# Kernel tuning notes

Hardware: AMD Instinct MI355X
Metric: run time of the kernel (lower is better)

Reference implementation:

```python
import jax, jax.numpy as jnp
import numpy as np

N_NODES = 100000
DEG = 16          # regular-graph degree so degrees[start] > 0 for all nodes
STEPS = 32
D_FEAT = 16
MAXI32 = 2147483647


def setup_inputs() -> dict:
    key = jax.random.key(0)
    k1, k2, k3 = jax.random.split(key, 3)
    x = jax.random.normal(k1, (N_NODES, D_FEAT), dtype=jnp.float32)
    # CSR-style flat adjacency list: node v's neighbors are
    # adj_nodes[adj_offset[v] : adj_offset[v] + degrees[v]]
    adj_nodes = jax.random.randint(k2, (N_NODES * DEG,), 0, N_NODES, dtype=jnp.int32)
    adj_offset = (jnp.arange(N_NODES, dtype=jnp.int32) * DEG)
    degrees = jnp.full((N_NODES,), DEG, dtype=jnp.int32)
    # cache of random integers, one per (step, walk), as in the torch code
    choices = jax.random.randint(k3, (STEPS, N_NODES), 0, MAXI32, dtype=jnp.int32)
    return {"x": x, "adj_nodes": adj_nodes, "adj_offset": adj_offset,
            "degrees": degrees, "choices": choices}


def reference(x, adj_nodes, adj_offset, degrees, choices):
    """Non-backtracking random walk (Walker.sample_walks with start_p=1.0,
    all nodes having degree > 0, so start = arange(n)).
    Returns walks [steps+1, w] and walk_edges [steps, w]."""
    n = degrees.shape[0]
    nb_degrees = jnp.maximum(degrees - 1, 1)  # reduced degree for non-backtrack rewrite
    start = jnp.arange(n, dtype=jnp.int32)

    def step(carry, ch):
        prev, cur = carry                      # [w] previous / current nodes
        deg = degrees[cur]
        edge_idx = ch % deg                    # unweighted modulo edge choice
        chosen = adj_offset[cur] + edge_idx
        new = adj_nodes[chosen]
        bt = new == prev                       # backtracking walks
        # conditional rewrite: pick a different outgoing edge
        alt = adj_offset[cur] + (edge_idx + 1 + ch % nb_degrees[cur]) % deg
        chosen = jnp.where(bt, alt, chosen)
        new = jnp.where(bt, adj_nodes[alt], new)
        return (cur, new), (new, chosen)

    # prev = -1 at step 0 => bt is all-False, matching the i > 0 guard
    prev0 = jnp.full_like(start, -1)
    _, (nodes, walk_edges) = jax.lax.scan(step, (prev0, start), choices)
    walks = jnp.concatenate([start[None, :], nodes], axis=0)  # [steps+1, w]
    return walks, walk_edges
```

## Files before the change

### kernel.cpp

```cpp
#include <hip/hip_runtime.h>


#define DEG 16
#define CHAINS 2
#define NMAX 131072
#define PACK_BLOCK 256
#define ENT_MASK 0x3FFFFu

__device__ unsigned int g_pk32[(size_t)NMAX * 9 + 2];
__device__ int g_flag;

__global__ __launch_bounds__(PACK_BLOCK) void pack_check_kernel(
    const int* __restrict__ adj_nodes,
    const int* __restrict__ adj_offset,
    const int* __restrict__ degrees,
    int n, int epoch) {
    __shared__ __align__(16) unsigned int lds[PACK_BLOCK * 9];

    int tid = threadIdx.x;
    int blockStart = blockIdx.x * PACK_BLOCK;
    int v = blockStart + tid;

    bool bad = false;
    if (v < n) {
        bad = (degrees[v] != DEG) || (adj_offset[v] != v * DEG);

        const uint4* row4 = (const uint4*)(adj_nodes + (size_t)v * DEG);
        uint4 r[4];
        r[0] = row4[0]; r[1] = row4[1]; r[2] = row4[2]; r[3] = row4[3];
        const unsigned* rr = (const unsigned*)r;

        unsigned dw[9];
#pragma unroll
        for (int j = 0; j < 9; ++j) dw[j] = 0u;
#pragma unroll
        for (int e = 0; e < 16; ++e) {
            unsigned id = rr[e];
            if (id >= 262144u) bad = true;
            unsigned s   = 18u * (unsigned)e;
            unsigned d   = s >> 5;
            unsigned off = s & 31u;
            dw[d] |= id << off;
            if (off > 14u) dw[d + 1] |= id >> (32u - off);
        }
#pragma unroll
        for (int e = 0; e < 16; ++e) {
            unsigned s   = 18u * (unsigned)e;
            unsigned d   = s >> 5;
            unsigned off = s & 31u;
            unsigned hi  = (off > 14u) ? dw[d + 1] : 0u;
            unsigned id  = __builtin_amdgcn_alignbit(hi, dw[d], off) & ENT_MASK;
            if (id != rr[e]) bad = true;
        }
#pragma unroll
        for (int j = 0; j < 9; ++j) lds[tid * 9 + j] = dw[j];
    }
    __syncthreads();

    int rows = n - blockStart;
    if (rows > PACK_BLOCK) rows = PACK_BLOCK;
    unsigned int* dstBase = g_pk32 + (size_t)blockStart * 9;
    if (rows == PACK_BLOCK) {
        uint4* dst4 = (uint4*)dstBase;
        const uint4* src4 = (const uint4*)lds;
        for (int i = tid; i < (PACK_BLOCK * 9) / 4; i += PACK_BLOCK)
            dst4[i] = src4[i];
    } else {
        int ndw = rows * 9;
        for (int i = tid; i < ndw; i += PACK_BLOCK) dstBase[i] = lds[i];
    }

    if (bad) g_flag = epoch;
}

template <int STEPS>
__global__ __launch_bounds__(64) void walker_fast5(
    const int* __restrict__ choices,
    int* __restrict__ out, int n, int h, int epoch,
    const int* __restrict__ adj_nodes,
    const int* __restrict__ adj_offset,
    const int* __restrict__ degrees) {

    int t = blockIdx.x * blockDim.x + threadIdx.x;
    if (t >= h) return;

    int* walks      = out;
    int* walk_edges = out + (STEPS + 1) * n;

    int w0 = t;
    int w1 = t + h;
    bool has1 = (w1 < n);
    int w1s = has1 ? w1 : w0;

    __builtin_nontemporal_store(w0, &walks[w0]);
    if (has1) __builtin_nontemporal_store(w1, &walks[w1]);

    if (g_flag != epoch) {
        int c0[STEPS], c1[STEPS];
#pragma unroll
        for (int i = 0; i < STEPS; ++i) {
            c0[i] = __builtin_nontemporal_load(&choices[i * n + w0]);
            c1[i] = __builtin_nontemporal_load(&choices[i * n + w1s]);
        }

        int prev0 = -1, cur0 = w0;
        int prev1 = -1, cur1 = w1s;
#pragma unroll
        for (int i = 0; i < STEPS; ++i) {
            unsigned ch0 = (unsigned)c0[i];
            unsigned ch1 = (unsigned)c1[i];
            unsigned e0 = ch0 & (DEG - 1);
            unsigned e1 = ch1 & (DEG - 1);
            unsigned a0 = (e0 + 1u + ch0 % (DEG - 1)) & (DEG - 1);
            unsigned a1 = (e1 + 1u + ch1 % (DEG - 1)) & (DEG - 1);

            const unsigned* row0 = g_pk32 + (size_t)(unsigned)cur0 * 9u;
            const unsigned* row1 = g_pk32 + (size_t)(unsigned)cur1 * 9u;

            unsigned s0 = 18u * e0, d0 = s0 >> 5, f0 = s0 & 31u;
            unsigned s1 = 18u * e1, d1 = s1 >> 5, f1 = s1 & 31u;
            unsigned sa = 18u * a0, da = sa >> 5, fa = sa & 31u;
            unsigned sb = 18u * a1, db = sb >> 5, fb = sb & 31u;

            uint2 q0 = *(const uint2*)(row0 + d0);
            uint2 qa = *(const uint2*)(row0 + da);
            uint2 q1 = *(const uint2*)(row1 + d1);
            uint2 qb = *(const uint2*)(row1 + db);

            int n00 = (int)(__builtin_amdgcn_alignbit(q0.y, q0.x, f0) & ENT_MASK);
            int n0a = (int)(__builtin_amdgcn_alignbit(qa.y, qa.x, fa) & ENT_MASK);
            int n10 = (int)(__builtin_amdgcn_alignbit(q1.y, q1.x, f1) & ENT_MASK);
            int n1b = (int)(__builtin_amdgcn_alignbit(qb.y, qb.x, fb) & ENT_MASK);

            bool bt0 = (n00 == prev0);
            bool bt1 = (n10 == prev1);
            int nw0 = bt0 ? n0a : n00;
            int nw1 = bt1 ? n1b : n10;
            unsigned ef0 = bt0 ? a0 : e0;
            unsigned ef1 = bt1 ? a1 : e1;

            int ce0 = (cur0 << 4) + (int)ef0;
            int ce1 = (cur1 << 4) + (int)ef1;

            __builtin_nontemporal_store(nw0, &walks[(i + 1) * n + w0]);
            __builtin_nontemporal_store(ce0, &walk_edges[i * n + w0]);
            if (has1) {
                __builtin_nontemporal_store(nw1, &walks[(i + 1) * n + w1]);
                __builtin_nontemporal_store(ce1, &walk_edges[i * n + w1]);
            }
            prev0 = cur0; cur0 = nw0;
            prev1 = cur1; cur1 = nw1;
        }
    } else {
        for (int k = 0; k < 2; ++k) {
            int w = (k == 0) ? w0 : w1;
            if (w >= n) break;
            int prev = -1, cur = w;
            for (int i = 0; i < STEPS; ++i) {
                int chv = choices[i * n + w];
                int deg = degrees[cur];
                int off = adj_offset[cur];
                int nb  = deg - 1 > 1 ? deg - 1 : 1;

                int e      = chv % deg;
                int chosen = off + e;
                int alt    = off + (e + 1 + chv % nb) % deg;

                int nv0 = adj_nodes[chosen];
                int nv1 = adj_nodes[alt];

                bool bt = (nv0 == prev);
                int nw  = bt ? nv1 : nv0;
                walks[(i + 1) * n + w] = nw;
                walk_edges[i * n + w]  = bt ? alt : chosen;
                prev = cur;
                cur  = nw;
            }
        }
    }
}

__global__ __launch_bounds__(256) void walker_generic(
    const int* __restrict__ adj_nodes,
    const int* __restrict__ adj_offset,
    const int* __restrict__ degrees,
    const int* __restrict__ choices,
    int* __restrict__ out, int n, int steps) {

    int w = blockIdx.x * blockDim.x + threadIdx.x;
    if (w >= n) return;

    int* walks      = out;
    int* walk_edges = out + (steps + 1) * n;
    walks[w] = w;

    int prev = -1, cur = w;
    for (int i = 0; i < steps; ++i) {
        int chv = choices[i * n + w];
        int deg = degrees[cur];
        int off = adj_offset[cur];
        int nb  = deg - 1 > 1 ? deg - 1 : 1;

        int e      = chv % deg;
        int chosen = off + e;
        int alt    = off + (e + 1 + chv % nb) % deg;

        int nv0 = adj_nodes[chosen];
        int nv1 = adj_nodes[alt];

        bool bt = (nv0 == prev);
        int nw  = bt ? nv1 : nv0;
        walks[(i + 1) * n + w] = nw;
        walk_edges[i * n + w]  = bt ? alt : chosen;
        prev = cur;
        cur  = nw;
    }
}

extern "C" void kernel_launch(void* const* d_in, const int* in_sizes, int n_in,
                              void* d_out, int out_size, void* d_ws, size_t ws_size,
                              hipStream_t stream) {
    const int* adj_nodes  = (const int*)d_in[1];
    const int* adj_offset = (const int*)d_in[2];
    const int* degrees    = (const int*)d_in[3];
    const int* choices    = (const int*)d_in[4];
    int* out = (int*)d_out;

    int n     = in_sizes[2];
    int steps = in_sizes[4] / n;

    if (steps == 32 && n <= NMAX) {
        static int s_epoch = 0;
        int epoch = ++s_epoch;

        int pg = (n + PACK_BLOCK - 1) / PACK_BLOCK;
        pack_check_kernel<<<pg, PACK_BLOCK, 0, stream>>>(adj_nodes, adj_offset,
                                                         degrees, n, epoch);

        int h  = (n + CHAINS - 1) / CHAINS;
        int wb = 64, wg = (h + wb - 1) / wb;
        walker_fast5<32><<<wg, wb, 0, stream>>>(choices, out, n, h, epoch,
                                                adj_nodes, adj_offset, degrees);
    } else {
        int block = 256, grid = (n + block - 1) / block;
        walker_generic<<<grid, block, 0, stream>>>(adj_nodes, adj_offset,
                                                   degrees, choices, out, n, steps);
    }
}
```

Measured before the change: 105.4 us.

## Use one walk per thread with lazy alternate-edge load and rolling choice prefetch

Replaces the two-walks-per-thread kernel with one walk per thread in 256-thread blocks, doubling the thread count. Choices are no longer preloaded into a 32-entry register array; each step prefetches only the next one. The alternate-edge load and modulo-15 are now done only when the chosen neighbour equals the previous node. This cuts registers and redundant gathers to raise occupancy, but gives up the two independent dependency chains per thread that hid gather latency.

```diff
diff --git a/kernel.cpp b/kernel.cpp
--- a/kernel.cpp
+++ b/kernel.cpp
@@ -2,7 +2,6 @@
 
 
 #define DEG 16
-#define CHAINS 2
 #define NMAX 131072
 #define PACK_BLOCK 256
 #define ENT_MASK 0x3FFFFu
@@ -74,108 +73,72 @@
 }
 
 template <int STEPS>
-__global__ __launch_bounds__(64) void walker_fast5(
+__global__ __launch_bounds__(256) void walker_fast6(
     const int* __restrict__ choices,
-    int* __restrict__ out, int n, int h, int epoch,
+    int* __restrict__ out, int n, int epoch,
     const int* __restrict__ adj_nodes,
     const int* __restrict__ adj_offset,
     const int* __restrict__ degrees) {
 
-    int t = blockIdx.x * blockDim.x + threadIdx.x;
-    if (t >= h) return;
+    int w = blockIdx.x * blockDim.x + threadIdx.x;
+    if (w >= n) return;
 
     int* walks      = out;
     int* walk_edges = out + (STEPS + 1) * n;
 
-    int w0 = t;
-    int w1 = t + h;
-    bool has1 = (w1 < n);
-    int w1s = has1 ? w1 : w0;
-
-    __builtin_nontemporal_store(w0, &walks[w0]);
-    if (has1) __builtin_nontemporal_store(w1, &walks[w1]);
+    __builtin_nontemporal_store(w, &walks[w]);
 
     if (g_flag != epoch) {
-        int c0[STEPS], c1[STEPS];
+        int prev = -1, cur = w;
+        int ch_next = __builtin_nontemporal_load(&choices[w]);
 #pragma unroll
         for (int i = 0; i < STEPS; ++i) {
-            c0[i] = __builtin_nontemporal_load(&choices[i * n + w0]);
-            c1[i] = __builtin_nontemporal_load(&choices[i * n + w1s]);
-        }
-
-        int prev0 = -1, cur0 = w0;
-        int prev1 = -1, cur1 = w1s;
-#pragma unroll
+            unsigned ch = (unsigned)ch_next;
+            if (i + 1 < STEPS)
+                ch_next = __builtin_nontemporal_load(&choices[(i + 1) * n + w]);
+
+            unsigned e = ch & (DEG - 1);
+            const unsigned* row = g_pk32 + (size_t)(unsigned)cur * 9u;
+            unsigned s = 18u * e, d = s >> 5, f = s & 31u;
+
+            uint2 q = *(const uint2*)(row + d);
+            int cand = (int)(__builtin_amdgcn_alignbit(q.y, q.x, f) & ENT_MASK);
+
+            int nw = cand;
+            unsigned ef = e;
+            if (cand == prev) {
+                unsigned a  = (e + 1u + ch % (DEG - 1)) & (DEG - 1);
+                unsigned sa = 18u * a, da = sa >> 5, fa = sa & 31u;
+                uint2 qa = *(const uint2*)(row + da);
+                nw = (int)(__builtin_amdgcn_alignbit(qa.y, qa.x, fa) & ENT_MASK);
+                ef = a;
+            }
+
+            __builtin_nontemporal_store(nw, &walks[(i + 1) * n + w]);
+            __builtin_nontemporal_store((cur << 4) + (int)ef, &walk_edges[i * n + w]);
+            prev = cur; cur = nw;
+        }
+    } else {
+        int prev = -1, cur = w;
         for (int i = 0; i < STEPS; ++i) {
-            unsigned ch0 = (unsigned)c0[i];
-            unsigned ch1 = (unsigned)c1[i];
-            unsigned e0 = ch0 & (DEG - 1);
-            unsigned e1 = ch1 & (DEG - 1);
-            unsigned a0 = (e0 + 1u + ch0 % (DEG - 1)) & (DEG - 1);
-            unsigned a1 = (e1 + 1u + ch1 % (DEG - 1)) & (DEG - 1);
-
-            const unsigned* row0 = g_pk32 + (size_t)(unsigned)cur0 * 9u;
-            const unsigned* row1 = g_pk32 + (size_t)(unsigned)cur1 * 9u;
-
-            unsigned s0 = 18u * e0, d0 = s0 >> 5, f0 = s0 & 31u;
-            unsigned s1 = 18u * e1, d1 = s1 >> 5, f1 = s1 & 31u;
-            unsigned sa = 18u * a0, da = sa >> 5, fa = sa & 31u;
-            unsigned sb = 18u * a1, db = sb >> 5, fb = sb & 31u;
-
-            uint2 q0 = *(const uint2*)(row0 + d0);
-            uint2 qa = *(const uint2*)(row0 + da);
-            uint2 q1 = *(const uint2*)(row1 + d1);
-            uint2 qb = *(const uint2*)(row1 + db);
-
-            int n00 = (int)(__builtin_amdgcn_alignbit(q0.y, q0.x, f0) & ENT_MASK);
-            int n0a = (int)(__builtin_amdgcn_alignbit(qa.y, qa.x, fa) & ENT_MASK);
-            int n10 = (int)(__builtin_amdgcn_alignbit(q1.y, q1.x, f1) & ENT_MASK);
-            int n1b = (int)(__builtin_amdgcn_alignbit(qb.y, qb.x, fb) & ENT_MASK);
-
-            bool bt0 = (n00 == prev0);
-            bool bt1 = (n10 == prev1);
-            int nw0 = bt0 ? n0a : n00;
-            int nw1 = bt1 ? n1b : n10;
-            unsigned ef0 = bt0 ? a0 : e0;
-            unsigned ef1 = bt1 ? a1 : e1;
-
-            int ce0 = (cur0 << 4) + (int)ef0;
-            int ce1 = (cur1 << 4) + (int)ef1;
-
-            __builtin_nontemporal_store(nw0, &walks[(i + 1) * n + w0]);
-            __builtin_nontemporal_store(ce0, &walk_edges[i * n + w0]);
-            if (has1) {
-                __builtin_nontemporal_store(nw1, &walks[(i + 1) * n + w1]);
-                __builtin_nontemporal_store(ce1, &walk_edges[i * n + w1]);
-            }
-            prev0 = cur0; cur0 = nw0;
-            prev1 = cur1; cur1 = nw1;
-        }
-    } else {
-        for (int k = 0; k < 2; ++k) {
-            int w = (k == 0) ? w0 : w1;
-            if (w >= n) break;
-            int prev = -1, cur = w;
-            for (int i = 0; i < STEPS; ++i) {
-                int chv = choices[i * n + w];
-                int deg = degrees[cur];
-                int off = adj_offset[cur];
-                int nb  = deg - 1 > 1 ? deg - 1 : 1;
-
-                int e      = chv % deg;
-                int chosen = off + e;
-                int alt    = off + (e + 1 + chv % nb) % deg;
-
-                int nv0 = adj_nodes[chosen];
-                int nv1 = adj_nodes[alt];
-
-                bool bt = (nv0 == prev);
-                int nw  = bt ? nv1 : nv0;
-                walks[(i + 1) * n + w] = nw;
-                walk_edges[i * n + w]  = bt ? alt : chosen;
-                prev = cur;
-                cur  = nw;
-            }
+            int chv = choices[i * n + w];
+            int deg = degrees[cur];
+            int off = adj_offset[cur];
+            int nb  = deg - 1 > 1 ? deg - 1 : 1;
+
+            int e      = chv % deg;
+            int chosen = off + e;
+            int alt    = off + (e + 1 + chv % nb) % deg;
+
+            int nv0 = adj_nodes[chosen];
+            int nv1 = adj_nodes[alt];
+
+            bool bt = (nv0 == prev);
+            int nw  = bt ? nv1 : nv0;
+            walks[(i + 1) * n + w] = nw;
+            walk_edges[i * n + w]  = bt ? alt : chosen;
+            prev = cur;
+            cur  = nw;
         }
     }
 }
@@ -237,9 +200,8 @@
         pack_check_kernel<<<pg, PACK_BLOCK, 0, stream>>>(adj_nodes, adj_offset,
                                                          degrees, n, epoch);
 
-        int h  = (n + CHAINS - 1) / CHAINS;
-        int wb = 64, wg = (h + wb - 1) / wb;
-        walker_fast5<32><<<wg, wb, 0, stream>>>(choices, out, n, h, epoch,
+        int wb = 256, wg = (n + wb - 1) / wb;
+        walker_fast6<32><<<wg, wb, 0, stream>>>(choices, out, n, epoch,
                                                 adj_nodes, adj_offset, degrees);
     } else {
         int block = 256, grid = (n + block - 1) / block;
```

Result: slower. 113.6 us (+7.8%).
